# Kernel tuning notes

Hardware: AMD Instinct MI355X
Metric: run time of the kernel (lower is better)

Reference implementation:

```python
import jax, jax.numpy as jnp
import numpy as np

NEG_SLOPE = 0.2


def gat_conv(x, src, dst, W, att_src, att_dst, bias, heads, out_ch, concat):
    # PyG GATConv (add_self_loops handled by caller). x: [N, in], W: [heads*out, in]
    N = x.shape[0]
    xw = (x @ W.T).reshape(N, heads, out_ch)                  # [N, H, C]
    a_src = jnp.sum(xw * att_src, axis=-1)                    # [N, H]
    a_dst = jnp.sum(xw * att_dst, axis=-1)                    # [N, H]
    alpha = a_src[src] + a_dst[dst]                           # [E, H]
    alpha = jax.nn.leaky_relu(alpha, NEG_SLOPE)
    # segment softmax over incoming edges of each dst node
    amax = jax.ops.segment_max(alpha, dst, num_segments=N)    # [N, H]
    amax = jnp.where(jnp.isfinite(amax), amax, 0.0)
    e = jnp.exp(alpha - amax[dst])                            # [E, H]
    denom = jax.ops.segment_sum(e, dst, num_segments=N)       # [N, H]
    coef = e / (denom[dst] + 1e-16)                           # [E, H]
    msg = xw[src] * coef[..., None]                           # [E, H, C]
    out = jax.ops.segment_sum(msg, dst, num_segments=N)       # [N, H, C]
    if concat:
        out = out.reshape(N, heads * out_ch)
    else:
        out = out.mean(axis=1)
    return out + bias


def setup_inputs() -> dict:
    key = jax.random.key(0)
    ks = jax.random.split(key, 10)
    N, E, F_IN, H, C = 50000, 1600000, 128, 4, 32
    x = jax.random.normal(ks[0], (N, F_IN), dtype=jnp.float32)
    edge_index = jax.random.randint(ks[1], (2, E), 0, N, dtype=jnp.int64)
    s1 = 1.0 / np.sqrt(F_IN)
    W1 = jax.random.uniform(ks[2], (H * C, F_IN), jnp.float32, -s1, s1)
    att_src1 = jax.random.normal(ks[3], (1, H, C), jnp.float32) * 0.1
    att_dst1 = jax.random.normal(ks[4], (1, H, C), jnp.float32) * 0.1
    b1 = jnp.zeros((H * C,), jnp.float32)
    s2 = 1.0 / np.sqrt(H * C)
    W2 = jax.random.uniform(ks[5], (1, H * C), jnp.float32, -s2, s2)
    att_src2 = jax.random.normal(ks[6], (1, 1, 1), jnp.float32) * 0.1
    att_dst2 = jax.random.normal(ks[7], (1, 1, 1), jnp.float32) * 0.1
    b2 = jnp.zeros((1,), jnp.float32)
    return {"x": x, "edge_index": edge_index, "W1": W1, "att_src1": att_src1,
            "att_dst1": att_dst1, "b1": b1, "W2": W2, "att_src2": att_src2,
            "att_dst2": att_dst2, "b2": b2}


def reference(x, edge_index, W1, att_src1, att_dst1, b1, W2, att_src2, att_dst2, b2):
    N = x.shape[0]
    loops = jnp.arange(N, dtype=edge_index.dtype)
    src = jnp.concatenate([edge_index[0], loops])
    dst = jnp.concatenate([edge_index[1], loops])
    h = gat_conv(x, src, dst, W1, att_src1, att_dst1, b1, heads=4, out_ch=32, concat=True)
    h = jax.nn.relu(h)
    out = gat_conv(h, src, dst, W2, att_src2, att_dst2, b2, heads=1, out_ch=1, concat=False)
    return out.squeeze(-1)
```

## Files before the change

### kernel.cpp

```cpp
#include <hip/hip_runtime.h>
#include <hip/hip_bf16.h>
#include <hip/hip_fp16.h>
#include <cstdint>
#include <cstddef>
#include <math.h>

#define NEG_SLOPE 0.2f
#define SLOTS 96
#define BSHIFT 7
#define BCAP 5632
#define SCB 768

__device__ __forceinline__ float lrelu(float x) { return x > 0.f ? x : NEG_SLOPE * x; }


__global__ __launch_bounds__(256) void k_gemm_scatter(
    const float* __restrict__ x, const float* __restrict__ W1,
    const float* __restrict__ att_src, const float* __restrict__ att_dst,
    const int* __restrict__ ei, int E, int N, int GB,
    __half* __restrict__ xw, float* __restrict__ a_src, float* __restrict__ a_dst,
    int* __restrict__ bin_cnt, unsigned* __restrict__ binned)
{
    __shared__ float As[32 * 68];
    __shared__ float Bs[32 * 132];

    if (blockIdx.x >= GB) {
        const int Et = E + N;
        const int nbin = (N + 127) >> BSHIFT;
        int* lhist = (int*)As;
        int* lbase = lhist + nbin;
        int* lpos  = lbase + nbin;
        const int bi = blockIdx.x - GB;
        const int chunk = (Et + SCB - 1) / SCB;
        const int e0 = bi * chunk;
        const int e1 = (e0 + chunk) < Et ? (e0 + chunk) : Et;
        for (int i = threadIdx.x; i < nbin; i += 256) { lhist[i] = 0; lpos[i] = 0; }
        __syncthreads();
        for (int e = e0 + threadIdx.x; e < e1; e += 256) {
            int d = (e < E) ? ei[(size_t)E + e] : (e - E);
            atomicAdd(&lhist[d >> BSHIFT], 1);
        }
        __syncthreads();
        for (int i = threadIdx.x; i < nbin; i += 256)
            lbase[i] = lhist[i] ? atomicAdd(&bin_cnt[i], lhist[i]) : 0;
        __syncthreads();
        for (int e = e0 + threadIdx.x; e < e1; e += 256) {
            int s, d;
            if (e < E) { s = ei[e]; d = ei[(size_t)E + e]; }
            else       { s = d = e - E; }
            int b = d >> BSHIFT;
            int p = lbase[b] + atomicAdd(&lpos[b], 1);
            if (p < BCAP)
                binned[(size_t)b * BCAP + p] =
                    ((unsigned)(d & 127) << 16) | (unsigned)s;
        }
        return;
    }

    const int tid = threadIdx.x;
    const int tx = tid & 31, ty = tid >> 5;
    const int bm = blockIdx.x * 64;
    float acc[8][4] = {};

    for (int k0 = 0; k0 < 128; k0 += 32) {
        #pragma unroll
        for (int t = tid; t < 512; t += 256) {
            int r = t >> 3, q = t & 7;
            int n = bm + r;
            float4 f = make_float4(0.f, 0.f, 0.f, 0.f);
            if (n < N) f = *(const float4*)(x + (size_t)n * 128 + k0 + 4 * q);
            As[(4*q+0)*68 + r] = f.x; As[(4*q+1)*68 + r] = f.y;
            As[(4*q+2)*68 + r] = f.z; As[(4*q+3)*68 + r] = f.w;
        }
        #pragma unroll
        for (int t = tid; t < 1024; t += 256) {
            int c = t >> 3, q = t & 7;
            float4 f = *(const float4*)(W1 + (size_t)c * 128 + k0 + 4 * q);
            Bs[(4*q+0)*132 + c] = f.x; Bs[(4*q+1)*132 + c] = f.y;
            Bs[(4*q+2)*132 + c] = f.z; Bs[(4*q+3)*132 + c] = f.w;
        }
        __syncthreads();
        #pragma unroll 8
        for (int kk = 0; kk < 32; kk++) {
            float4 a0 = *(const float4*)&As[kk * 68 + ty * 8];
            float4 a1 = *(const float4*)&As[kk * 68 + ty * 8 + 4];
            float4 b4 = *(const float4*)&Bs[kk * 132 + tx * 4];
            float a[8] = {a0.x, a0.y, a0.z, a0.w, a1.x, a1.y, a1.z, a1.w};
            float b[4] = {b4.x, b4.y, b4.z, b4.w};
            #pragma unroll
            for (int i = 0; i < 8; i++)
                #pragma unroll
                for (int j = 0; j < 4; j++) acc[i][j] = fmaf(a[i], b[j], acc[i][j]);
        }
        __syncthreads();
    }

    float asv[4], adv[4];
    #pragma unroll
    for (int j = 0; j < 4; j++) { asv[j] = att_src[tx*4+j]; adv[j] = att_dst[tx*4+j]; }
    const int head = tx >> 3;

    #pragma unroll
    for (int i = 0; i < 8; i++) {
        int n = bm + ty * 8 + i;
        float sv = 0.f, dv = 0.f;
        #pragma unroll
        for (int j = 0; j < 4; j++) {
            sv = fmaf(acc[i][j], asv[j], sv);
            dv = fmaf(acc[i][j], adv[j], dv);
        }
        #pragma unroll
        for (int off = 1; off < 8; off <<= 1) {
            sv += __shfl_xor(sv, off);
            dv += __shfl_xor(dv, off);
        }
        if (n < N) {
            __half2 h0 = __floats2half2_rn(acc[i][0], acc[i][1]);
            __half2 h1 = __floats2half2_rn(acc[i][2], acc[i][3]);
            float2 st;
            ((__half2*)&st)[0] = h0;
            ((__half2*)&st)[1] = h1;
            *(float2*)(xw + (size_t)n * 128 + tx * 4) = st;
            if ((tx & 7) == 0) {
                a_src[n * 4 + head] = sv;
                a_dst[n * 4 + head] = dv;
            }
        }
    }
}

__global__ __launch_bounds__(256) void k_bin2bucket(
    const unsigned* __restrict__ binned, const int* __restrict__ bin_cnt,
    int* __restrict__ cnt, unsigned short* __restrict__ bucket, int N)
{
    __shared__ int lcnt[128];
    __shared__ unsigned short lb[128][SLOTS];
    const int b = blockIdx.x;
    const int base_d = b << BSHIFT;
    for (int i = threadIdx.x; i < 128; i += 256) lcnt[i] = 0;
    __syncthreads();
    int bc = bin_cnt[b]; bc = bc < BCAP ? bc : BCAP;
    const unsigned* src = binned + (size_t)b * BCAP;
    for (int t = threadIdx.x; t < bc; t += 256) {
        unsigned w = src[t];
        int dl = (int)(w >> 16);
        int p = atomicAdd(&lcnt[dl], 1);
        if (p < SLOTS) lb[dl][p] = (unsigned short)(w & 0xFFFFu);
    }
    __syncthreads();
    for (int dl = threadIdx.x; dl < 128; dl += 256) {
        int d = base_d + dl;
        if (d >= N) continue;
        int deg = lcnt[dl]; deg = deg < SLOTS ? deg : SLOTS;
        cnt[d] = deg;
        unsigned* go = (unsigned*)(bucket + (size_t)d * SLOTS);
        const unsigned* lrow = (const unsigned*)lb[dl];
        int nw = (deg + 1) >> 1;
        for (int i = 0; i < nw; i++) go[i] = lrow[i];
    }
}

__global__ __launch_bounds__(256) void k_agg(const __half* __restrict__ xw,
                                             const float* __restrict__ a_src,
                                             const float* __restrict__ a_dst,
                                             const int* __restrict__ cnt,
                                             const unsigned short* __restrict__ bucket,
                                             const float* __restrict__ b1,
                                             const float* __restrict__ W2,
                                             float* __restrict__ xw2, int N)
{
    const int wv = threadIdx.x >> 6, lane = threadIdx.x & 63;
    const int es = lane >> 4, cl = lane & 15;
    const int d = blockIdx.x * 4 + wv;
    if (d >= N) return;
    const int head = cl >> 2;
    int deg = cnt[d]; deg = deg < SLOTS ? deg : SLOTS;
    const unsigned short* brow = bucket + (size_t)d * SLOTS;

    float4 ad4 = ((const float4*)a_dst)[d];
    float adh = (head & 2) ? ((head & 1) ? ad4.w : ad4.z)
                           : ((head & 1) ? ad4.y : ad4.x);

    float acc[8] = {};
    float csum = 0.f;
    const int j0 = 2 * es, j1 = 2 * es + 1;
    for (int k = 0; k < deg; k += 8) {
        ushort2 ss = *(const ushort2*)(brow + k + 2 * es);
        bool v0 = (k + j0) < deg;
        bool v1 = (k + j1) < deg;
        int s0 = v0 ? (int)ss.x : 0;
        int s1 = v1 ? (int)ss.y : 0;
        float4 as0 = ((const float4*)a_src)[s0];
        float4 as1 = ((const float4*)a_src)[s1];
        float4 x0 = *(const float4*)(xw + (size_t)s0 * 128 + cl * 8);
        float4 x1 = *(const float4*)(xw + (size_t)s1 * 128 + cl * 8);
        float ash0 = (head & 2) ? ((head & 1) ? as0.w : as0.z)
                                : ((head & 1) ? as0.y : as0.x);
        float ash1 = (head & 2) ? ((head & 1) ? as1.w : as1.z)
                                : ((head & 1) ? as1.y : as1.x);
        float c0 = v0 ? __expf(lrelu(ash0 + adh)) : 0.f;
        float c1 = v1 ? __expf(lrelu(ash1 + adh)) : 0.f;
        const __half2* h0 = (const __half2*)&x0;
        const __half2* h1 = (const __half2*)&x1;
        #pragma unroll
        for (int q = 0; q < 4; q++) {
            float2 f0 = __half22float2(h0[q]);
            float2 f1 = __half22float2(h1[q]);
            acc[2*q]   = fmaf(c0, f0.x, acc[2*q]);
            acc[2*q+1] = fmaf(c0, f0.y, acc[2*q+1]);
            acc[2*q]   = fmaf(c1, f1.x, acc[2*q]);
            acc[2*q+1] = fmaf(c1, f1.y, acc[2*q+1]);
        }
        csum += c0 + c1;
    }
    #pragma unroll
    for (int q = 0; q < 8; q++) {
        acc[q] += __shfl_xor(acc[q], 16);
        acc[q] += __shfl_xor(acc[q], 32);
    }
    csum += __shfl_xor(csum, 16);
    csum += __shfl_xor(csum, 32);

    float inv = 1.f / (csum + 1e-16f);
    float4 bb0 = ((const float4*)b1)[cl * 2], bb1 = ((const float4*)b1)[cl * 2 + 1];
    float4 ww0 = ((const float4*)W2)[cl * 2], ww1 = ((const float4*)W2)[cl * 2 + 1];
    float t = fmaxf(fmaf(acc[0], inv, bb0.x), 0.f) * ww0.x
            + fmaxf(fmaf(acc[1], inv, bb0.y), 0.f) * ww0.y
            + fmaxf(fmaf(acc[2], inv, bb0.z), 0.f) * ww0.z
            + fmaxf(fmaf(acc[3], inv, bb0.w), 0.f) * ww0.w
            + fmaxf(fmaf(acc[4], inv, bb1.x), 0.f) * ww1.x
            + fmaxf(fmaf(acc[5], inv, bb1.y), 0.f) * ww1.y
            + fmaxf(fmaf(acc[6], inv, bb1.z), 0.f) * ww1.z
            + fmaxf(fmaf(acc[7], inv, bb1.w), 0.f) * ww1.w;
    #pragma unroll
    for (int off = 1; off < 16; off <<= 1) t += __shfl_xor(t, off);
    if (lane == 0) xw2[d] = t;
}

__global__ __launch_bounds__(256) void k_layer2(const float* __restrict__ xw2,
                                                const int* __restrict__ cnt,
                                                const unsigned short* __restrict__ bucket,
                                                const float* __restrict__ att_src2,
                                                const float* __restrict__ att_dst2,
                                                const float* __restrict__ b2,
                                                float* __restrict__ out, int N)
{
    int grpi = (blockIdx.x * blockDim.x + threadIdx.x) >> 6;
    int lane = threadIdx.x & 63;
    int sub  = lane >> 4, li = lane & 15;
    int d    = grpi * 4 + sub;
    if (d >= N) return;
    float as2  = att_src2[0];
    float adst = xw2[d] * att_dst2[0];
    int deg = cnt[d]; deg = deg < SLOTS ? deg : SLOTS;
    const unsigned short* brow = bucket + (size_t)d * SLOTS;
    float l = 0.f, acc = 0.f;
    for (int j = li; j < deg; j += 16) {
        int s = brow[j];
        float xs = xw2[s];
        float p = __expf(lrelu(fmaf(xs, as2, adst)));
        l += p;
        acc = fmaf(p, xs, acc);
    }
    #pragma unroll
    for (int off = 1; off < 16; off <<= 1) {
        l   += __shfl_xor(l, off);
        acc += __shfl_xor(acc, off);
    }
    if (li == 0) out[d] = acc / (l + 1e-16f) + b2[0];
}

extern "C" void kernel_launch(void* const* d_in, const int* in_sizes, int n_in,
                              void* d_out, int out_size, void* d_ws, size_t ws_size,
                              hipStream_t stream)
{
    const float* x        = (const float*)d_in[0];
    const int*   ei       = (const int*)d_in[1];
    const float* W1       = (const float*)d_in[2];
    const float* att_src1 = (const float*)d_in[3];
    const float* att_dst1 = (const float*)d_in[4];
    const float* b1       = (const float*)d_in[5];
    const float* W2       = (const float*)d_in[6];
    const float* att_src2 = (const float*)d_in[7];
    const float* att_dst2 = (const float*)d_in[8];
    const float* b2       = (const float*)d_in[9];
    float* out = (float*)d_out;

    const int N  = in_sizes[0] / 128;
    const int E  = in_sizes[1] / 2;
    const int NBIN = (N + 127) >> BSHIFT;

    char* p = (char*)d_ws;
    auto alloc = [&](size_t bytes) {
        char* r = p;
        p += (bytes + 255) & ~(size_t)255;
        return (void*)r;
    };
    __half* xw    = (__half*)alloc((size_t)N * 128 * 2);
    float* a_src  = (float*)alloc((size_t)N * 4 * 4);
    float* a_dst  = (float*)alloc((size_t)N * 4 * 4);
    float* xw2    = (float*)alloc((size_t)N * 4);
    int*   cnt    = (int*)alloc((size_t)N * 4);
    unsigned short* bucket = (unsigned short*)alloc((size_t)N * SLOTS * 2);
    unsigned* binned = (unsigned*)alloc((size_t)NBIN * BCAP * 4);
    int* bin_cnt  = (int*)alloc((size_t)NBIN * 4);

    (void)hipMemsetAsync(bin_cnt, 0, (size_t)NBIN * 4, stream);

    const int GB = (N + 63) / 64;
    k_gemm_scatter<<<GB + SCB, 256, 0, stream>>>(x, W1, att_src1, att_dst1, ei, E, N,
                                                 GB, xw, a_src, a_dst, bin_cnt, binned);
    k_bin2bucket  <<<NBIN,       256, 0, stream>>>(binned, bin_cnt, cnt, bucket, N);
    k_agg         <<<(N + 3)/4,  256, 0, stream>>>(xw, a_src, a_dst, cnt, bucket,
                                                   b1, W2, xw2, N);
    k_layer2      <<<(N + 15)/16, 256, 0, stream>>>(xw2, cnt, bucket, att_src2,
                                                    att_dst2, b2, out, N);
}
```

Before: 210.2 us.

## Compute layer-1 projection with fp16 MFMA and stage output through LDS

```diff
diff --git a/kernel.cpp b/kernel.cpp
--- a/kernel.cpp
+++ b/kernel.cpp
@@ -11,23 +11,35 @@
 #define BCAP 5632
 #define SCB 768
 
+typedef __attribute__((ext_vector_type(8))) _Float16 f16x8;
+typedef __attribute__((ext_vector_type(4))) float f32x4;
+
 __device__ __forceinline__ float lrelu(float x) { return x > 0.f ? x : NEG_SLOPE * x; }
 
 
+__global__ __launch_bounds__(256) void k_init(const float* __restrict__ W1,
+                                              __half* __restrict__ W1h,
+                                              int* __restrict__ bin_cnt, int nbin)
+{
+    int i = blockIdx.x * 256 + threadIdx.x;
+    if (i < 128 * 128) W1h[i] = (__half)W1[i];
+    if (i < nbin) bin_cnt[i] = 0;
+}
+
 __global__ __launch_bounds__(256) void k_gemm_scatter(
-    const float* __restrict__ x, const float* __restrict__ W1,
+    const float* __restrict__ x, const __half* __restrict__ W1h,
     const float* __restrict__ att_src, const float* __restrict__ att_dst,
     const int* __restrict__ ei, int E, int N, int GB,
     __half* __restrict__ xw, float* __restrict__ a_src, float* __restrict__ a_dst,
     int* __restrict__ bin_cnt, unsigned* __restrict__ binned)
 {
-    __shared__ float As[32 * 68];
-    __shared__ float Bs[32 * 132];
+    __shared__ __half tile[64][136];
+    __shared__ float s_as[128], s_ad[128];
 
     if (blockIdx.x >= GB) {
         const int Et = E + N;
         const int nbin = (N + 127) >> BSHIFT;
-        int* lhist = (int*)As;
+        int* lhist = (int*)tile;
         int* lbase = lhist + nbin;
         int* lpos  = lbase + nbin;
         const int bi = blockIdx.x - GB;
@@ -58,73 +70,74 @@
     }
 
     const int tid = threadIdx.x;
-    const int tx = tid & 31, ty = tid >> 5;
+    if (tid < 128) { s_as[tid] = att_src[tid]; s_ad[tid] = att_dst[tid]; }
+
+    const int wv = tid >> 6, lane = tid & 63;
+    const int rl = lane & 15, g = lane >> 4;
     const int bm = blockIdx.x * 64;
-    float acc[8][4] = {};
-
+    const int row = bm + wv * 16 + rl;
+    const int rr = row < N ? row : N - 1;
+    const float* xr = x + (size_t)rr * 128 + g * 8;
+
+    f32x4 acc[8];
+    #pragma unroll
+    for (int i = 0; i < 8; i++) acc[i] = (f32x4){0.f, 0.f, 0.f, 0.f};
+
+    #pragma unroll
     for (int k0 = 0; k0 < 128; k0 += 32) {
+        float4 fa0 = *(const float4*)(xr + k0);
+        float4 fa1 = *(const float4*)(xr + k0 + 4);
+        f16x8 a;
+        a[0] = (_Float16)fa0.x; a[1] = (_Float16)fa0.y;
+        a[2] = (_Float16)fa0.z; a[3] = (_Float16)fa0.w;
+        a[4] = (_Float16)fa1.x; a[5] = (_Float16)fa1.y;
+        a[6] = (_Float16)fa1.z; a[7] = (_Float16)fa1.w;
         #pragma unroll
-        for (int t = tid; t < 512; t += 256) {
-            int r = t >> 3, q = t & 7;
-            int n = bm + r;
-            float4 f = make_float4(0.f, 0.f, 0.f, 0.f);
-            if (n < N) f = *(const float4*)(x + (size_t)n * 128 + k0 + 4 * q);
-            As[(4*q+0)*68 + r] = f.x; As[(4*q+1)*68 + r] = f.y;
-            As[(4*q+2)*68 + r] = f.z; As[(4*q+3)*68 + r] = f.w;
-        }
+        for (int ct = 0; ct < 8; ct++) {
+            f16x8 b = *(const f16x8*)(W1h + (size_t)(ct * 16 + rl) * 128 + k0 + g * 8);
+            acc[ct] = __builtin_amdgcn_mfma_f32_16x16x32_f16(a, b, acc[ct], 0, 0, 0);
+        }
+    }
+    #pragma unroll
+    for (int ct = 0; ct < 8; ct++)
         #pragma unroll
-        for (int t = tid; t < 1024; t += 256) {
-            int c = t >> 3, q = t & 7;
-            float4 f = *(const float4*)(W1 + (size_t)c * 128 + k0 + 4 * q);
-            Bs[(4*q+0)*132 + c] = f.x; Bs[(4*q+1)*132 + c] = f.y;
-            Bs[(4*q+2)*132 + c] = f.z; Bs[(4*q+3)*132 + c] = f.w;
-        }
-        __syncthreads();
-        #pragma unroll 8
-        for (int kk = 0; kk < 32; kk++) {
-            float4 a0 = *(const float4*)&As[kk * 68 + ty * 8];
-            float4 a1 = *(const float4*)&As[kk * 68 + ty * 8 + 4];
-            float4 b4 = *(const float4*)&Bs[kk * 132 + tx * 4];
-            float a[8] = {a0.x, a0.y, a0.z, a0.w, a1.x, a1.y, a1.z, a1.w};
-            float b[4] = {b4.x, b4.y, b4.z, b4.w};
+        for (int r = 0; r < 4; r++)
+            tile[wv * 16 + g * 4 + r][ct * 16 + rl] = (__half)acc[ct][r];
+    __syncthreads();
+
+    {
+        int r = tid >> 2, h = tid & 3;
+        int n = bm + r;
+        if (n < N) {
+            float4 vv[4];
+            vv[0] = *(const float4*)&tile[r][h * 32];
+            vv[1] = *(const float4*)&tile[r][h * 32 + 8];
+            vv[2] = *(const float4*)&tile[r][h * 32 + 16];
+            vv[3] = *(const float4*)&tile[r][h * 32 + 24];
+            __half* xo = xw + (size_t)n * 128 + h * 32;
+            *(float4*)(xo)      = vv[0];
+            *(float4*)(xo + 8)  = vv[1];
+            *(float4*)(xo + 16) = vv[2];
+            *(float4*)(xo + 24) = vv[3];
+            const float4* asp = (const float4*)(s_as + h * 32);
+            const float4* adp = (const float4*)(s_ad + h * 32);
+            float sv = 0.f, dv = 0.f;
             #pragma unroll
-            for (int i = 0; i < 8; i++)
-                #pragma unroll
-                for (int j = 0; j < 4; j++) acc[i][j] = fmaf(a[i], b[j], acc[i][j]);
-        }
-        __syncthreads();
-    }
-
-    float asv[4], adv[4];
-    #pragma unroll
-    for (int j = 0; j < 4; j++) { asv[j] = att_src[tx*4+j]; adv[j] = att_dst[tx*4+j]; }
-    const int head = tx >> 3;
-
-    #pragma unroll
-    for (int i = 0; i < 8; i++) {
-        int n = bm + ty * 8 + i;
-        float sv = 0.f, dv = 0.f;
-        #pragma unroll
-        for (int j = 0; j < 4; j++) {
-            sv = fmaf(acc[i][j], asv[j], sv);
-            dv = fmaf(acc[i][j], adv[j], dv);
-        }
-        #pragma unroll
-        for (int off = 1; off < 8; off <<= 1) {
-            sv += __shfl_xor(sv, off);
-            dv += __shfl_xor(dv, off);
-        }
-        if (n < N) {
-            __half2 h0 = __floats2half2_rn(acc[i][0], acc[i][1]);
-            __half2 h1 = __floats2half2_rn(acc[i][2], acc[i][3]);
-            float2 st;
-            ((__half2*)&st)[0] = h0;
-            ((__half2*)&st)[1] = h1;
-            *(float2*)(xw + (size_t)n * 128 + tx * 4) = st;
-            if ((tx & 7) == 0) {
-                a_src[n * 4 + head] = sv;
-                a_dst[n * 4 + head] = dv;
+            for (int q = 0; q < 4; q++) {
+                const __half2* hp = (const __half2*)&vv[q];
+                float2 f0 = __half22float2(hp[0]);
+                float2 f1 = __half22float2(hp[1]);
+                float2 f2 = __half22float2(hp[2]);
+                float2 f3 = __half22float2(hp[3]);
+                float4 A0 = asp[2 * q], A1 = asp[2 * q + 1];
+                float4 D0 = adp[2 * q], D1 = adp[2 * q + 1];
+                sv += f0.x * A0.x + f0.y * A0.y + f1.x * A0.z + f1.y * A0.w
+                    + f2.x * A1.x + f2.y * A1.y + f3.x * A1.z + f3.y * A1.w;
+                dv += f0.x * D0.x + f0.y * D0.y + f1.x * D0.z + f1.y * D0.w
+                    + f2.x * D1.x + f2.y * D1.y + f3.x * D1.z + f3.y * D1.w;
             }
+            a_src[n * 4 + h] = sv;
+            a_dst[n * 4 + h] = dv;
         }
     }
 }
@@ -297,6 +310,7 @@
         return (void*)r;
     };
     __half* xw    = (__half*)alloc((size_t)N * 128 * 2);
+    __half* W1h   = (__half*)alloc((size_t)128 * 128 * 2);
     float* a_src  = (float*)alloc((size_t)N * 4 * 4);
     float* a_dst  = (float*)alloc((size_t)N * 4 * 4);
     float* xw2    = (float*)alloc((size_t)N * 4);
@@ -305,14 +319,14 @@
     unsigned* binned = (unsigned*)alloc((size_t)NBIN * BCAP * 4);
     int* bin_cnt  = (int*)alloc((size_t)NBIN * 4);
 
-    (void)hipMemsetAsync(bin_cnt, 0, (size_t)NBIN * 4, stream);
-
     const int GB = (N + 63) / 64;
-    k_gemm_scatter<<<GB + SCB, 256, 0, stream>>>(x, W1, att_src1, att_dst1, ei, E, N,
-                                                 GB, xw, a_src, a_dst, bin_cnt, binned);
-    k_bin2bucket  <<<NBIN,       256, 0, stream>>>(binned, bin_cnt, cnt, bucket, N);
-    k_agg         <<<(N + 3)/4,  256, 0, stream>>>(xw, a_src, a_dst, cnt, bucket,
-                                                   b1, W2, xw2, N);
+    k_init        <<<64,          256, 0, stream>>>(W1, W1h, bin_cnt, NBIN);
+    k_gemm_scatter<<<GB + SCB,    256, 0, stream>>>(x, W1h, att_src1, att_dst1, ei,
+                                                    E, N, GB, xw, a_src, a_dst,
+                                                    bin_cnt, binned);
+    k_bin2bucket  <<<NBIN,        256, 0, stream>>>(binned, bin_cnt, cnt, bucket, N);
+    k_agg         <<<(N + 3)/4,   256, 0, stream>>>(xw, a_src, a_dst, cnt, bucket,
+                                                    b1, W2, xw2, N);
     k_layer2      <<<(N + 15)/16, 256, 0, stream>>>(xw2, cnt, bucket, att_src2,
                                                     att_dst2, b2, out, N);
 }
```

Measured after the change: 202.5 us. -3.6%, faster.
